# Optimization experiments

Measured on AMD Instinct MI355X. Metric: run time of the kernel, lower is better.

## Reference

```python
import jax, jax.numpy as jnp
import numpy as np

N_NODES = 100000
N_EDGES = 800000
IN_DIM = 128
HID = 128
N_CLASSES = 4


def setup_inputs() -> dict:
    key = jax.random.key(0)
    ks = jax.random.split(key, 8)
    x = jax.random.normal(ks[0], (N_NODES, IN_DIM), dtype=jnp.float32)
    edge_index = jax.random.randint(ks[1], (2, N_EDGES), 0, N_NODES, dtype=jnp.int32)
    s0 = 1.0 / np.sqrt(IN_DIM)
    s1 = 1.0 / np.sqrt(HID)
    W0 = jax.random.uniform(ks[2], (HID, IN_DIM), minval=-s0, maxval=s0, dtype=jnp.float32)
    b0 = jax.random.uniform(ks[3], (HID,), minval=-s0, maxval=s0, dtype=jnp.float32)
    W1 = jax.random.uniform(ks[4], (HID, HID), minval=-s1, maxval=s1, dtype=jnp.float32)
    b1 = jax.random.uniform(ks[5], (HID,), minval=-s1, maxval=s1, dtype=jnp.float32)
    Wc = jax.random.uniform(ks[6], (N_CLASSES, HID), minval=-s1, maxval=s1, dtype=jnp.float32)
    bc = jax.random.uniform(ks[7], (N_CLASSES,), minval=-s1, maxval=s1, dtype=jnp.float32)
    return {"x": x, "edge_index": edge_index, "W0": W0, "b0": b0,
            "W1": W1, "b1": b1, "Wc": Wc, "bc": bc}


def reference(x, edge_index, W0, b0, W1, b1, Wc, bc):
    row, col = edge_index[0], edge_index[1]
    n = x.shape[0]
    # layer 0: Linear + ReLU (dropout is identity in eval)
    h = jax.nn.relu(x @ W0.T + b0)                                  # [N, HID]
    # scatter-add neighbor aggregation with degree normalization
    agg = jax.ops.segment_sum(h[col], row, num_segments=n)          # [N, HID]
    deg = jax.ops.segment_sum(jnp.ones_like(row, dtype=h.dtype), row, num_segments=n)
    agg = agg / jnp.clip(deg, 1.0)[:, None]
    h = h + agg                                                     # residual add
    # final conv + ReLU + classifier
    h = jax.nn.relu(h @ W1.T + b1)
    logits = h @ Wc.T + bc                                          # [N, N_CLASSES]
    return logits
```

## Files before the change

### kernel.cpp

```cpp
#include <hip/hip_runtime.h>

#define IN_DIM 128
#define HID    128
#define NCLS   4

typedef __attribute__((ext_vector_type(8))) short bf16x8;
typedef __attribute__((ext_vector_type(4))) float f32x4;

__device__ inline ushort f2bf(float x) {
    uint u = __builtin_bit_cast(uint, x);
    u += 0x7FFFu + ((u >> 16) & 1u);
    return (ushort)(u >> 16);
}
__device__ inline float bf2f(ushort h) {
    uint u = ((uint)h) << 16;
    return __builtin_bit_cast(float, u);
}

__global__ __launch_bounds__(256) void cast_x(const float* __restrict__ X,
                                              ushort* __restrict__ hi,
                                              ushort* __restrict__ lo,
                                              int n, int npad)
{
    int i = blockIdx.x * 256 + threadIdx.x;
    if (i * 4 >= npad) return;
    float4 v = make_float4(0.f, 0.f, 0.f, 0.f);
    if (i * 4 < n) v = ((const float4*)X)[i];
    ushort4 h4, l4;
    h4.x = f2bf(v.x); l4.x = f2bf(v.x - bf2f(h4.x));
    h4.y = f2bf(v.y); l4.y = f2bf(v.y - bf2f(h4.y));
    h4.z = f2bf(v.z); l4.z = f2bf(v.z - bf2f(h4.z));
    h4.w = f2bf(v.w); l4.w = f2bf(v.w - bf2f(h4.w));
    ((ushort4*)hi)[i] = h4;
    ((ushort4*)lo)[i] = l4;
}

__global__ __launch_bounds__(256) void cast_w(const float* __restrict__ W0,
                                              const float* __restrict__ W1,
                                              ushort* __restrict__ w0h, ushort* __restrict__ w0l,
                                              ushort* __restrict__ w1h, ushort* __restrict__ w1l)
{
    int i = blockIdx.x * 256 + threadIdx.x;
    float v = (i < 16384) ? W0[i] : W1[i - 16384];
    ushort h = f2bf(v);
    ushort l = f2bf(v - bf2f(h));
    if (i < 16384) { w0h[i] = h; w0l[i] = l; }
    else           { w1h[i - 16384] = h; w1l[i - 16384] = l; }
}

__device__ inline void mfma_main(const ushort* __restrict__ Ahi, const ushort* __restrict__ Alo,
                                 const ushort* __restrict__ Whi, const ushort* __restrict__ Wlo,
                                 int rowbase, int colbase, int lr, int lk,
                                 f32x4 acc[2][4])
{
    #pragma unroll
    for (int kt = 0; kt < 4; ++kt) {
        const int ko = kt * 32 + lk * 8;
        bf16x8 ah[2], al[2];
        #pragma unroll
        for (int rt = 0; rt < 2; ++rt) {
            size_t ao = (size_t)(rowbase + rt * 16 + lr) * 128 + ko;
            ah[rt] = *(const bf16x8*)(Ahi + ao);
            al[rt] = *(const bf16x8*)(Alo + ao);
        }
        #pragma unroll
        for (int nt = 0; nt < 4; ++nt) {
            size_t bo = (size_t)(colbase + nt * 16 + lr) * 128 + ko;
            bf16x8 bh = *(const bf16x8*)(Whi + bo);
            bf16x8 bl = *(const bf16x8*)(Wlo + bo);
            #pragma unroll
            for (int rt = 0; rt < 2; ++rt) {
                acc[rt][nt] = __builtin_amdgcn_mfma_f32_16x16x32_bf16(ah[rt], bh, acc[rt][nt], 0, 0, 0);
                acc[rt][nt] = __builtin_amdgcn_mfma_f32_16x16x32_bf16(ah[rt], bl, acc[rt][nt], 0, 0, 0);
                acc[rt][nt] = __builtin_amdgcn_mfma_f32_16x16x32_bf16(al[rt], bh, acc[rt][nt], 0, 0, 0);
            }
        }
    }
}

__global__ __launch_bounds__(256) void gnn_lin0_mfma(const ushort* __restrict__ Xhi,
                                                     const ushort* __restrict__ Xlo,
                                                     const ushort* __restrict__ Whi,
                                                     const ushort* __restrict__ Wlo,
                                                     const float* __restrict__ Bv,
                                                     float* __restrict__ H, int M)
{
    const int tid = threadIdx.x;
    const int wid = tid >> 6, lane = tid & 63;
    const int wr = wid >> 1, wc = wid & 1;
    const int rowbase = blockIdx.x * 64 + wr * 32;
    const int colbase = wc * 64;
    const int lr = lane & 15, lk = lane >> 4;

    f32x4 acc[2][4];
    #pragma unroll
    for (int rt = 0; rt < 2; ++rt)
        #pragma unroll
        for (int nt = 0; nt < 4; ++nt) acc[rt][nt] = (f32x4){0.f, 0.f, 0.f, 0.f};

    mfma_main(Xhi, Xlo, Whi, Wlo, rowbase, colbase, lr, lk, acc);

    #pragma unroll
    for (int nt = 0; nt < 4; ++nt) {
        const int col = colbase + nt * 16 + lr;
        const float bv = Bv[col];
        #pragma unroll
        for (int rt = 0; rt < 2; ++rt) {
            #pragma unroll
            for (int r = 0; r < 4; ++r) {
                int row = rowbase + rt * 16 + lk * 4 + r;
                if (row < M)
                    H[(size_t)row * 128 + col] = fmaxf(acc[rt][nt][r] + bv, 0.f);
            }
        }
    }
}

__global__ __launch_bounds__(256) void gnn_lin1_mfma(const ushort* __restrict__ Ahi,
                                                     const ushort* __restrict__ Alo,
                                                     const ushort* __restrict__ Whi,
                                                     const ushort* __restrict__ Wlo,
                                                     const float* __restrict__ Bv,
                                                     const float* __restrict__ Wc,
                                                     const float* __restrict__ bc,
                                                     float* __restrict__ Out, int M)
{
    __shared__ float red[256 * 33];

    const int tid = threadIdx.x;
    const int wid = tid >> 6, lane = tid & 63;
    const int wr = wid >> 1, wc = wid & 1;
    const int rowbase = blockIdx.x * 64 + wr * 32;
    const int colbase = wc * 64;
    const int lr = lane & 15, lk = lane >> 4;

    f32x4 acc[2][4];
    #pragma unroll
    for (int rt = 0; rt < 2; ++rt)
        #pragma unroll
        for (int nt = 0; nt < 4; ++nt) acc[rt][nt] = (f32x4){0.f, 0.f, 0.f, 0.f};

    mfma_main(Ahi, Alo, Whi, Wlo, rowbase, colbase, lr, lk, acc);

    f32x4 p[2][4];
    #pragma unroll
    for (int rt = 0; rt < 2; ++rt)
        #pragma unroll
        for (int r = 0; r < 4; ++r) p[rt][r] = (f32x4){0.f, 0.f, 0.f, 0.f};

    #pragma unroll
    for (int nt = 0; nt < 4; ++nt) {
        const int col = colbase + nt * 16 + lr;
        const float bv = Bv[col];
        f32x4 wcv = { Wc[col], Wc[128 + col], Wc[256 + col], Wc[384 + col] };
        #pragma unroll
        for (int rt = 0; rt < 2; ++rt)
            #pragma unroll
            for (int r = 0; r < 4; ++r) {
                float h2 = fmaxf(acc[rt][nt][r] + bv, 0.f);
                p[rt][r] += wcv * h2;
            }
    }

    #pragma unroll
    for (int rt = 0; rt < 2; ++rt)
        #pragma unroll
        for (int r = 0; r < 4; ++r)
            #pragma unroll
            for (int c = 0; c < 4; ++c)
                red[tid * 33 + rt * 16 + r * 4 + c] = p[rt][r][c];
    __syncthreads();

    const int row_local = tid >> 2, cls = tid & 3;
    const int wr2 = row_local >> 5, rt2 = (row_local >> 4) & 1;
    const int lg = (row_local >> 2) & 3, reg = row_local & 3;
    float s = bc[cls];
    #pragma unroll
    for (int w2 = 0; w2 < 2; ++w2)
        #pragma unroll
        for (int i = 0; i < 16; ++i) {
            int lane_lin = (wr2 * 2 + w2) * 64 + lg * 16 + i;
            s += red[lane_lin * 33 + rt2 * 16 + reg * 4 + cls];
        }
    int row = blockIdx.x * 64 + row_local;
    if (row < M) Out[(size_t)row * 4 + cls] = s;
}

__global__ __launch_bounds__(256) void count_deg(const int* __restrict__ rows,
                                                 int* __restrict__ deg, int E)
{
    int e = blockIdx.x * 256 + threadIdx.x;
    if (e < E) atomicAdd(&deg[rows[e]], 1);
}

__global__ __launch_bounds__(256) void scan_blocks(const int* __restrict__ deg,
                                                   int* __restrict__ off,
                                                   int* __restrict__ bsum, int M)
{
    __shared__ int sh[256];
    int i = blockIdx.x * 256 + threadIdx.x;
    int v = (i < M) ? deg[i] : 0;
    sh[threadIdx.x] = v;
    __syncthreads();
    #pragma unroll
    for (int d = 1; d < 256; d <<= 1) {
        int t = (threadIdx.x >= d) ? sh[threadIdx.x - d] : 0;
        __syncthreads();
        sh[threadIdx.x] += t;
        __syncthreads();
    }
    if (i < M) off[i] = sh[threadIdx.x] - v;
    if (threadIdx.x == 255) bsum[blockIdx.x] = sh[255];
}

__global__ __launch_bounds__(512) void scan_bsum(int* __restrict__ bsum, int NB)
{
    __shared__ int sh[512];
    int v = (threadIdx.x < NB) ? bsum[threadIdx.x] : 0;
    sh[threadIdx.x] = v;
    __syncthreads();
    #pragma unroll
    for (int d = 1; d < 512; d <<= 1) {
        int t = (threadIdx.x >= d) ? sh[threadIdx.x - d] : 0;
        __syncthreads();
        sh[threadIdx.x] += t;
        __syncthreads();
    }
    if (threadIdx.x < NB) bsum[threadIdx.x] = sh[threadIdx.x] - v;
}

__global__ __launch_bounds__(256) void add_off(int* __restrict__ off,
                                               const int* __restrict__ bsum,
                                               int* __restrict__ pos, int M)
{
    int i = blockIdx.x * 256 + threadIdx.x;
    if (i < M) {
        int o = off[i] + bsum[i >> 8];
        off[i] = o;
        pos[i] = o;
    }
}

__global__ __launch_bounds__(256) void fill_csr(const int* __restrict__ rows,
                                                const int* __restrict__ cols,
                                                int* __restrict__ pos,
                                                int* __restrict__ col_sorted, int E)
{
    int e = blockIdx.x * 256 + threadIdx.x;
    if (e < E) {
        int p = atomicAdd(&pos[rows[e]], 1);
        col_sorted[p] = cols[e];
    }
}

__global__ __launch_bounds__(256) void gnn_aggregate(const float* __restrict__ H,
                                                     const int* __restrict__ off,
                                                     const int* __restrict__ deg,
                                                     const int* __restrict__ col_sorted,
                                                     ushort* __restrict__ AggHi,
                                                     ushort* __restrict__ AggLo,
                                                     int M, int Mpad)
{
    int gid  = blockIdx.x * 8 + (threadIdx.x >> 5);
    int lane = threadIdx.x & 31;
    if (gid >= Mpad) return;
    size_t oidx = (size_t)gid * 32 + lane;
    if (gid >= M) {
        ((ushort4*)AggHi)[oidx] = make_ushort4(0, 0, 0, 0);
        ((ushort4*)AggLo)[oidx] = make_ushort4(0, 0, 0, 0);
        return;
    }

    const float4* H4 = (const float4*)H;
    int start = off[gid];
    int d     = deg[gid];

    float4 acc = make_float4(0.f, 0.f, 0.f, 0.f);
    for (int e = start; e < start + d; ++e) {
        int c = col_sorted[e];
        float4 v = H4[(size_t)c * 32 + lane];
        acc.x += v.x; acc.y += v.y; acc.z += v.z; acc.w += v.w;
    }
    float inv = 1.0f / fmaxf((float)d, 1.0f);
    float4 hv = H4[(size_t)gid * 32 + lane];
    float o0 = hv.x + acc.x * inv;
    float o1 = hv.y + acc.y * inv;
    float o2 = hv.z + acc.z * inv;
    float o3 = hv.w + acc.w * inv;

    ushort4 h4, l4;
    h4.x = f2bf(o0); l4.x = f2bf(o0 - bf2f(h4.x));
    h4.y = f2bf(o1); l4.y = f2bf(o1 - bf2f(h4.y));
    h4.z = f2bf(o2); l4.z = f2bf(o2 - bf2f(h4.z));
    h4.w = f2bf(o3); l4.w = f2bf(o3 - bf2f(h4.w));
    ((ushort4*)AggHi)[oidx] = h4;
    ((ushort4*)AggLo)[oidx] = l4;
}

extern "C" void kernel_launch(void* const* d_in, const int* in_sizes, int n_in,
                              void* d_out, int out_size, void* d_ws, size_t ws_size,
                              hipStream_t stream)
{
    const float* x  = (const float*)d_in[0];
    const int*   ei = (const int*)  d_in[1];
    const float* W0 = (const float*)d_in[2];
    const float* b0 = (const float*)d_in[3];
    const float* W1 = (const float*)d_in[4];
    const float* b1 = (const float*)d_in[5];
    const float* Wc = (const float*)d_in[6];
    const float* bc = (const float*)d_in[7];
    float* out = (float*)d_out;

    const int M    = in_sizes[0] / IN_DIM;
    const int E    = in_sizes[1] / 2;
    const int Mpad = (M + 63) & ~63;
    const int NB   = (M + 255) / 256;

    ushort* Xhi = (ushort*)d_ws;
    ushort* Xlo = Xhi + (size_t)Mpad * 128;
    float*  H   = (float*)(Xlo + (size_t)Mpad * 128);
    ushort* W0h = (ushort*)(H + (size_t)M * 128);
    ushort* W0l = W0h + 16384;
    ushort* W1h = W0l + 16384;
    ushort* W1l = W1h + 16384;
    int* deg_i  = (int*)(W1l + 16384);
    int* off    = deg_i + M;
    int* pos    = off + M;
    int* bsum   = pos + M;
    int* col_sorted = bsum + 512;

    const int* rows = ei;
    const int* cols = ei + E;

    hipMemsetAsync(deg_i, 0, (size_t)M * sizeof(int), stream);

    const int n    = M * IN_DIM;
    const int npad = Mpad * IN_DIM;
    const int gridCast = (npad / 4 + 255) / 256;
    const int gridMM   = Mpad / 64;
    const int gridE    = (E + 255) / 256;
    const int gridN    = (M + 255) / 256;

    cast_x<<<gridCast, 256, 0, stream>>>(x, Xhi, Xlo, n, npad);
    cast_w<<<128, 256, 0, stream>>>(W0, W1, W0h, W0l, W1h, W1l);
    gnn_lin0_mfma<<<gridMM, 256, 0, stream>>>(Xhi, Xlo, W0h, W0l, b0, H, M);

    count_deg<<<gridE, 256, 0, stream>>>(rows, deg_i, E);
    scan_blocks<<<gridN, 256, 0, stream>>>(deg_i, off, bsum, M);
    scan_bsum<<<1, 512, 0, stream>>>(bsum, NB);
    add_off<<<gridN, 256, 0, stream>>>(off, bsum, pos, M);
    fill_csr<<<gridE, 256, 0, stream>>>(rows, cols, pos, col_sorted, E);

    gnn_aggregate<<<(Mpad + 7) / 8, 256, 0, stream>>>(H, off, deg_i, col_sorted,
                                                      Xhi, Xlo, M, Mpad);
    gnn_lin1_mfma<<<gridMM, 256, 0, stream>>>(Xhi, Xlo, W1h, W1l, b1, Wc, bc, out, M);
}
```

Before: 355.7 us.

## Fuse x split into lin0, store H as bf16 hi/lo, gather bf16 only

Drops the separate cast_x kernel: lin0 now reads fp32 x directly and splits it into bf16 hi/lo in registers. lin0 writes H as a bf16 hi/lo pair instead of fp32. The aggregate kernel gathers only the bf16 hi part of each neighbour, halving gather bytes, and unrolls the edge loop by two with dual accumulators. The residual term is rebuilt from hi+lo, but the neighbour mean now uses reduced-precision features, which adds numerical error.

```diff
diff --git a/kernel.cpp b/kernel.cpp
--- a/kernel.cpp
+++ b/kernel.cpp
@@ -17,22 +17,15 @@
     return __builtin_bit_cast(float, u);
 }
 
-__global__ __launch_bounds__(256) void cast_x(const float* __restrict__ X,
-                                              ushort* __restrict__ hi,
-                                              ushort* __restrict__ lo,
-                                              int n, int npad)
-{
-    int i = blockIdx.x * 256 + threadIdx.x;
-    if (i * 4 >= npad) return;
-    float4 v = make_float4(0.f, 0.f, 0.f, 0.f);
-    if (i * 4 < n) v = ((const float4*)X)[i];
-    ushort4 h4, l4;
-    h4.x = f2bf(v.x); l4.x = f2bf(v.x - bf2f(h4.x));
-    h4.y = f2bf(v.y); l4.y = f2bf(v.y - bf2f(h4.y));
-    h4.z = f2bf(v.z); l4.z = f2bf(v.z - bf2f(h4.z));
-    h4.w = f2bf(v.w); l4.w = f2bf(v.w - bf2f(h4.w));
-    ((ushort4*)hi)[i] = h4;
-    ((ushort4*)lo)[i] = l4;
+__device__ inline void split8(const float4& x0, const float4& x1, bf16x8& h, bf16x8& l) {
+    float v[8] = {x0.x, x0.y, x0.z, x0.w, x1.x, x1.y, x1.z, x1.w};
+    #pragma unroll
+    for (int j = 0; j < 8; ++j) {
+        ushort hh = f2bf(v[j]);
+        ushort ll = f2bf(v[j] - bf2f(hh));
+        h[j] = (short)hh;
+        l[j] = (short)ll;
+    }
 }
 
 __global__ __launch_bounds__(256) void cast_w(const float* __restrict__ W0,
@@ -48,42 +41,12 @@
     else           { w1h[i - 16384] = h; w1l[i - 16384] = l; }
 }
 
-__device__ inline void mfma_main(const ushort* __restrict__ Ahi, const ushort* __restrict__ Alo,
-                                 const ushort* __restrict__ Whi, const ushort* __restrict__ Wlo,
-                                 int rowbase, int colbase, int lr, int lk,
-                                 f32x4 acc[2][4])
-{
-    #pragma unroll
-    for (int kt = 0; kt < 4; ++kt) {
-        const int ko = kt * 32 + lk * 8;
-        bf16x8 ah[2], al[2];
-        #pragma unroll
-        for (int rt = 0; rt < 2; ++rt) {
-            size_t ao = (size_t)(rowbase + rt * 16 + lr) * 128 + ko;
-            ah[rt] = *(const bf16x8*)(Ahi + ao);
-            al[rt] = *(const bf16x8*)(Alo + ao);
-        }
-        #pragma unroll
-        for (int nt = 0; nt < 4; ++nt) {
-            size_t bo = (size_t)(colbase + nt * 16 + lr) * 128 + ko;
-            bf16x8 bh = *(const bf16x8*)(Whi + bo);
-            bf16x8 bl = *(const bf16x8*)(Wlo + bo);
-            #pragma unroll
-            for (int rt = 0; rt < 2; ++rt) {
-                acc[rt][nt] = __builtin_amdgcn_mfma_f32_16x16x32_bf16(ah[rt], bh, acc[rt][nt], 0, 0, 0);
-                acc[rt][nt] = __builtin_amdgcn_mfma_f32_16x16x32_bf16(ah[rt], bl, acc[rt][nt], 0, 0, 0);
-                acc[rt][nt] = __builtin_amdgcn_mfma_f32_16x16x32_bf16(al[rt], bh, acc[rt][nt], 0, 0, 0);
-            }
-        }
-    }
-}
-
-__global__ __launch_bounds__(256) void gnn_lin0_mfma(const ushort* __restrict__ Xhi,
-                                                     const ushort* __restrict__ Xlo,
+__global__ __launch_bounds__(256) void gnn_lin0_mfma(const float* __restrict__ X,
                                                      const ushort* __restrict__ Whi,
                                                      const ushort* __restrict__ Wlo,
                                                      const float* __restrict__ Bv,
-                                                     float* __restrict__ H, int M)
+                                                     ushort* __restrict__ Hhi,
+                                                     ushort* __restrict__ Hlo, int M)
 {
     const int tid = threadIdx.x;
     const int wid = tid >> 6, lane = tid & 63;
@@ -98,7 +61,37 @@
         #pragma unroll
         for (int nt = 0; nt < 4; ++nt) acc[rt][nt] = (f32x4){0.f, 0.f, 0.f, 0.f};
 
-    mfma_main(Xhi, Xlo, Whi, Wlo, rowbase, colbase, lr, lk, acc);
+    const float4* X4 = (const float4*)X;
+
+    #pragma unroll
+    for (int kt = 0; kt < 4; ++kt) {
+        const int ko = kt * 32 + lk * 8;
+        bf16x8 ah[2], al[2];
+        #pragma unroll
+        for (int rt = 0; rt < 2; ++rt) {
+            int row = rowbase + rt * 16 + lr;
+            float4 x0 = make_float4(0.f, 0.f, 0.f, 0.f);
+            float4 x1 = x0;
+            if (row < M) {
+                size_t base = (size_t)row * 32 + (ko >> 2);
+                x0 = X4[base];
+                x1 = X4[base + 1];
+            }
+            split8(x0, x1, ah[rt], al[rt]);
+        }
+        #pragma unroll
+        for (int nt = 0; nt < 4; ++nt) {
+            size_t bo = (size_t)(colbase + nt * 16 + lr) * 128 + ko;
+            bf16x8 bh = *(const bf16x8*)(Whi + bo);
+            bf16x8 bl = *(const bf16x8*)(Wlo + bo);
+            #pragma unroll
+            for (int rt = 0; rt < 2; ++rt) {
+                acc[rt][nt] = __builtin_amdgcn_mfma_f32_16x16x32_bf16(ah[rt], bh, acc[rt][nt], 0, 0, 0);
+                acc[rt][nt] = __builtin_amdgcn_mfma_f32_16x16x32_bf16(ah[rt], bl, acc[rt][nt], 0, 0, 0);
+                acc[rt][nt] = __builtin_amdgcn_mfma_f32_16x16x32_bf16(al[rt], bh, acc[rt][nt], 0, 0, 0);
+            }
+        }
+    }
 
     #pragma unroll
     for (int nt = 0; nt < 4; ++nt) {
@@ -109,8 +102,14 @@
             #pragma unroll
             for (int r = 0; r < 4; ++r) {
                 int row = rowbase + rt * 16 + lk * 4 + r;
-                if (row < M)
-                    H[(size_t)row * 128 + col] = fmaxf(acc[rt][nt][r] + bv, 0.f);
+                if (row < M) {
+                    float o = fmaxf(acc[rt][nt][r] + bv, 0.f);
+                    ushort hh = f2bf(o);
+                    ushort ll = f2bf(o - bf2f(hh));
+                    size_t oo = (size_t)row * 128 + col;
+                    Hhi[oo] = hh;
+                    Hlo[oo] = ll;
+                }
             }
         }
     }
@@ -140,7 +139,29 @@
         #pragma unroll
         for (int nt = 0; nt < 4; ++nt) acc[rt][nt] = (f32x4){0.f, 0.f, 0.f, 0.f};
 
-    mfma_main(Ahi, Alo, Whi, Wlo, rowbase, colbase, lr, lk, acc);
+    #pragma unroll
+    for (int kt = 0; kt < 4; ++kt) {
+        const int ko = kt * 32 + lk * 8;
+        bf16x8 ah[2], al[2];
+        #pragma unroll
+        for (int rt = 0; rt < 2; ++rt) {
+            size_t ao = (size_t)(rowbase + rt * 16 + lr) * 128 + ko;
+            ah[rt] = *(const bf16x8*)(Ahi + ao);
+            al[rt] = *(const bf16x8*)(Alo + ao);
+        }
+        #pragma unroll
+        for (int nt = 0; nt < 4; ++nt) {
+            size_t bo = (size_t)(colbase + nt * 16 + lr) * 128 + ko;
+            bf16x8 bh = *(const bf16x8*)(Whi + bo);
+            bf16x8 bl = *(const bf16x8*)(Wlo + bo);
+            #pragma unroll
+            for (int rt = 0; rt < 2; ++rt) {
+                acc[rt][nt] = __builtin_amdgcn_mfma_f32_16x16x32_bf16(ah[rt], bh, acc[rt][nt], 0, 0, 0);
+                acc[rt][nt] = __builtin_amdgcn_mfma_f32_16x16x32_bf16(ah[rt], bl, acc[rt][nt], 0, 0, 0);
+                acc[rt][nt] = __builtin_amdgcn_mfma_f32_16x16x32_bf16(al[rt], bh, acc[rt][nt], 0, 0, 0);
+            }
+        }
+    }
 
     f32x4 p[2][4];
     #pragma unroll
@@ -253,12 +274,13 @@
     }
 }
 
-__global__ __launch_bounds__(256) void gnn_aggregate(const float* __restrict__ H,
+__global__ __launch_bounds__(256) void gnn_aggregate(const ushort* __restrict__ Hhi,
+                                                     const ushort* __restrict__ Hlo,
                                                      const int* __restrict__ off,
                                                      const int* __restrict__ deg,
                                                      const int* __restrict__ col_sorted,
-                                                     ushort* __restrict__ AggHi,
-                                                     ushort* __restrict__ AggLo,
+                                                     ushort* __restrict__ InHi,
+                                                     ushort* __restrict__ InLo,
                                                      int M, int Mpad)
 {
     int gid  = blockIdx.x * 8 + (threadIdx.x >> 5);
@@ -266,35 +288,49 @@
     if (gid >= Mpad) return;
     size_t oidx = (size_t)gid * 32 + lane;
     if (gid >= M) {
-        ((ushort4*)AggHi)[oidx] = make_ushort4(0, 0, 0, 0);
-        ((ushort4*)AggLo)[oidx] = make_ushort4(0, 0, 0, 0);
+        ((ushort4*)InHi)[oidx] = make_ushort4(0, 0, 0, 0);
+        ((ushort4*)InLo)[oidx] = make_ushort4(0, 0, 0, 0);
         return;
     }
 
-    const float4* H4 = (const float4*)H;
+    const ushort4* G = (const ushort4*)Hhi;
     int start = off[gid];
     int d     = deg[gid];
-
-    float4 acc = make_float4(0.f, 0.f, 0.f, 0.f);
-    for (int e = start; e < start + d; ++e) {
-        int c = col_sorted[e];
-        float4 v = H4[(size_t)c * 32 + lane];
-        acc.x += v.x; acc.y += v.y; acc.z += v.z; acc.w += v.w;
-    }
+    int end   = start + d;
+
+    float a0 = 0.f, a1 = 0.f, a2 = 0.f, a3 = 0.f;
+    float b0 = 0.f, b1 = 0.f, b2 = 0.f, b3 = 0.f;
+    int e = start;
+    for (; e + 2 <= end; e += 2) {
+        int c0 = col_sorted[e];
+        int c1 = col_sorted[e + 1];
+        ushort4 g0 = G[(size_t)c0 * 32 + lane];
+        ushort4 g1 = G[(size_t)c1 * 32 + lane];
+        a0 += bf2f(g0.x); a1 += bf2f(g0.y); a2 += bf2f(g0.z); a3 += bf2f(g0.w);
+        b0 += bf2f(g1.x); b1 += bf2f(g1.y); b2 += bf2f(g1.z); b3 += bf2f(g1.w);
+    }
+    if (e < end) {
+        int c0 = col_sorted[e];
+        ushort4 g0 = G[(size_t)c0 * 32 + lane];
+        a0 += bf2f(g0.x); a1 += bf2f(g0.y); a2 += bf2f(g0.z); a3 += bf2f(g0.w);
+    }
+    a0 += b0; a1 += b1; a2 += b2; a3 += b3;
+
     float inv = 1.0f / fmaxf((float)d, 1.0f);
-    float4 hv = H4[(size_t)gid * 32 + lane];
-    float o0 = hv.x + acc.x * inv;
-    float o1 = hv.y + acc.y * inv;
-    float o2 = hv.z + acc.z * inv;
-    float o3 = hv.w + acc.w * inv;
+    ushort4 rh = ((const ushort4*)Hhi)[oidx];
+    ushort4 rl = ((const ushort4*)Hlo)[oidx];
+    float o0 = bf2f(rh.x) + bf2f(rl.x) + a0 * inv;
+    float o1 = bf2f(rh.y) + bf2f(rl.y) + a1 * inv;
+    float o2 = bf2f(rh.z) + bf2f(rl.z) + a2 * inv;
+    float o3 = bf2f(rh.w) + bf2f(rl.w) + a3 * inv;
 
     ushort4 h4, l4;
     h4.x = f2bf(o0); l4.x = f2bf(o0 - bf2f(h4.x));
     h4.y = f2bf(o1); l4.y = f2bf(o1 - bf2f(h4.y));
     h4.z = f2bf(o2); l4.z = f2bf(o2 - bf2f(h4.z));
     h4.w = f2bf(o3); l4.w = f2bf(o3 - bf2f(h4.w));
-    ((ushort4*)AggHi)[oidx] = h4;
-    ((ushort4*)AggLo)[oidx] = l4;
+    ((ushort4*)InHi)[oidx] = h4;
+    ((ushort4*)InLo)[oidx] = l4;
 }
 
 extern "C" void kernel_launch(void* const* d_in, const int* in_sizes, int n_in,
@@ -316,17 +352,18 @@
     const int Mpad = (M + 63) & ~63;
     const int NB   = (M + 255) / 256;
 
-    ushort* Xhi = (ushort*)d_ws;
-    ushort* Xlo = Xhi + (size_t)Mpad * 128;
-    float*  H   = (float*)(Xlo + (size_t)Mpad * 128);
-    ushort* W0h = (ushort*)(H + (size_t)M * 128);
-    ushort* W0l = W0h + 16384;
-    ushort* W1h = W0l + 16384;
-    ushort* W1l = W1h + 16384;
-    int* deg_i  = (int*)(W1l + 16384);
-    int* off    = deg_i + M;
-    int* pos    = off + M;
-    int* bsum   = pos + M;
+    ushort* Hhi  = (ushort*)d_ws;
+    ushort* Hlo  = Hhi  + (size_t)Mpad * 128;
+    ushort* InHi = Hlo  + (size_t)Mpad * 128;
+    ushort* InLo = InHi + (size_t)Mpad * 128;
+    ushort* W0h  = InLo + (size_t)Mpad * 128;
+    ushort* W0l  = W0h + 16384;
+    ushort* W1h  = W0l + 16384;
+    ushort* W1l  = W1h + 16384;
+    int* deg_i   = (int*)(W1l + 16384);
+    int* off     = deg_i + M;
+    int* pos     = off + M;
+    int* bsum    = pos + M;
     int* col_sorted = bsum + 512;
 
     const int* rows = ei;
@@ -334,16 +371,12 @@
 
     hipMemsetAsync(deg_i, 0, (size_t)M * sizeof(int), stream);
 
-    const int n    = M * IN_DIM;
-    const int npad = Mpad * IN_DIM;
-    const int gridCast = (npad / 4 + 255) / 256;
-    const int gridMM   = Mpad / 64;
-    const int gridE    = (E + 255) / 256;
-    const int gridN    = (M + 255) / 256;
-
-    cast_x<<<gridCast, 256, 0, stream>>>(x, Xhi, Xlo, n, npad);
+    const int gridMM = Mpad / 64;
+    const int gridE  = (E + 255) / 256;
+    const int gridN  = (M + 255) / 256;
+
     cast_w<<<128, 256, 0, stream>>>(W0, W1, W0h, W0l, W1h, W1l);
-    gnn_lin0_mfma<<<gridMM, 256, 0, stream>>>(Xhi, Xlo, W0h, W0l, b0, H, M);
+    gnn_lin0_mfma<<<gridMM, 256, 0, stream>>>(x, W0h, W0l, b0, Hhi, Hlo, M);
 
     count_deg<<<gridE, 256, 0, stream>>>(rows, deg_i, E);
     scan_blocks<<<gridN, 256, 0, stream>>>(deg_i, off, bsum, M);
@@ -351,7 +384,7 @@
     add_off<<<gridN, 256, 0, stream>>>(off, bsum, pos, M);
     fill_csr<<<gridE, 256, 0, stream>>>(rows, cols, pos, col_sorted, E);
 
-    gnn_aggregate<<<(Mpad + 7) / 8, 256, 0, stream>>>(H, off, deg_i, col_sorted,
-                                                      Xhi, Xlo, M, Mpad);
-    gnn_lin1_mfma<<<gridMM, 256, 0, stream>>>(Xhi, Xlo, W1h, W1l, b1, Wc, bc, out, M);
-}
+    gnn_aggregate<<<(Mpad + 7) / 8, 256, 0, stream>>>(Hhi, Hlo, off, deg_i, col_sorted,
+                                                      InHi, InLo, M, Mpad);
+    gnn_lin1_mfma<<<gridMM, 256, 0, stream>>>(InHi, InLo, W1h, W1l, b1, Wc, bc, out, M);
+}
```

Measured after the change: 325.6 us. 8.5% less time.
